# Kernel tuning notes

Measured on AMD Instinct MI355X. Metric: run time of the kernel, lower is better.

Reference implementation:

```python
import jax, jax.numpy as jnp
import numpy as np
import math

B, C, T = 32, 512, 1024
QUERY_DIM = 512
SCALE = 1.0 / math.sqrt(QUERY_DIM)


def setup_inputs() -> dict:
    key = jax.random.key(0)
    ks = jax.random.split(key, 10)
    lim = 1.0 / math.sqrt(C)  # torch Linear default init range
    return {
        "x": jax.random.normal(ks[0], (B, C, T), dtype=jnp.float32),
        "g_query": jax.random.uniform(ks[1], (B, C, T), dtype=jnp.float32),
        "g_keys": jax.random.uniform(ks[2], (B, C, T), dtype=jnp.float32),
        "g_values": jax.random.uniform(ks[3], (B, C, T), dtype=jnp.float32),
        "Wq": jax.random.uniform(ks[4], (C, C), jnp.float32, -lim, lim),
        "bq": jax.random.uniform(ks[5], (C,), jnp.float32, -lim, lim),
        "Wk": jax.random.uniform(ks[6], (C, C), jnp.float32, -lim, lim),
        "bk": jax.random.uniform(ks[7], (C,), jnp.float32, -lim, lim),
        "Wv": jax.random.uniform(ks[8], (C, C), jnp.float32, -lim, lim),
        "bv": jax.random.uniform(ks[9], (C,), jnp.float32, -lim, lim),
    }


def reference(x, g_query, g_keys, g_values, Wq, bq, Wk, bk, Wv, bv):
    # x, gates: [B, C, T] -> transpose to [B, T, C]
    xt = jnp.swapaxes(x, 1, 2)
    gq = jnp.swapaxes(g_query, 1, 2)
    gk = jnp.swapaxes(g_keys, 1, 2)
    gv = jnp.swapaxes(g_values, 1, 2)
    # torch Linear: y = x @ W^T + b
    q = gq * (jnp.einsum('btc,dc->btd', xt, Wq) + bq)  # [B, T, C]
    k = gk * (jnp.einsum('btc,dc->btd', xt, Wk) + bk)  # [B, T, C]
    v = gv * (jnp.einsum('btc,dc->btd', xt, Wv) + bv)  # [B, T, C]
    # energy[b,c,d] = sum_t q[b,t,c] * k[b,t,d]  (channel-channel attention)
    energy = jnp.einsum('btc,btd->bcd', q, k)  # [B, C, C]
    attn = jax.nn.softmax(energy * SCALE, axis=2)
    # out[b,c,t] = sum_d attn[b,c,d] * v[b,t,d]
    out = jnp.einsum('bcd,btd->bct', attn, v)  # [B, C, T]
    return out
```

## Files before the change

kernel.cpp:

```cpp
#include <hip/hip_runtime.h>
#include <math.h>


#define B_ 32
#define C_ 512
#define T_ 1024
#define TC_ ((size_t)524288)
#define CC_ ((size_t)262144)
#define SCALE_ 0.04419417382415922f

typedef short bf16x8 __attribute__((ext_vector_type(8)));
typedef float f32x4 __attribute__((ext_vector_type(4)));

__device__ __forceinline__ unsigned short f2b(float f) {
    unsigned int u = __float_as_uint(f);
    u += 0x7fff + ((u >> 16) & 1);
    return (unsigned short)(u >> 16);
}
__device__ __forceinline__ float b2f(unsigned short h) {
    return __uint_as_float(((unsigned int)h) << 16);
}

#define GLDS(gp, lp) __builtin_amdgcn_global_load_lds( \
    (const __attribute__((address_space(1))) unsigned int*)(const void*)(gp), \
    (__attribute__((address_space(3))) unsigned int*)(void*)(lp), 16, 0, 0)

template<int M, int N, int K, int EP>
__global__ __launch_bounds__(256, 2) void gemm_nt(
    const unsigned short* __restrict__ Ahi, const unsigned short* __restrict__ Alo, size_t sA,
    const unsigned short* __restrict__ Bhi, const unsigned short* __restrict__ Blo, size_t sB,
    float* __restrict__ Cf, size_t sCf,
    unsigned short* __restrict__ Chi, unsigned short* __restrict__ Clo, size_t sC,
    const float* __restrict__ gate, size_t sG,
    const float* __restrict__ bias)
{
    __shared__ __attribute__((aligned(16))) unsigned short sAh[128 * 32];
    __shared__ __attribute__((aligned(16))) unsigned short sAl[128 * 32];
    __shared__ __attribute__((aligned(16))) unsigned short sBh[128 * 32];
    __shared__ __attribute__((aligned(16))) unsigned short sBl[128 * 32];

    const int tid  = threadIdx.x;
    const int lane = tid & 63;
    const int wave = tid >> 6;
    const int bz   = blockIdx.z;
    const int m0   = blockIdx.y * 128;
    const int n0   = blockIdx.x * 128;

    const unsigned short* pAh = Ahi + (size_t)bz * sA;
    const unsigned short* pAl = Alo + (size_t)bz * sA;
    const unsigned short* pBh = Bhi + (size_t)bz * sB;
    const unsigned short* pBl = Blo + (size_t)bz * sB;

    const int srow = wave * 32;
    const int lr   = lane >> 2;
    const int lk   = (lane & 3) * 8;
    const size_t gA0 = (size_t)(m0 + srow + lr) * K + lk;
    const size_t gA1 = (size_t)(m0 + srow + 16 + lr) * K + lk;
    const size_t gB0 = (size_t)(n0 + srow + lr) * K + lk;
    const size_t gB1 = (size_t)(n0 + srow + 16 + lr) * K + lk;
    unsigned short* lds0 = nullptr;  (void)lds0;

    const int wm = (wave & 1) * 64;
    const int wn = (wave >> 1) * 64;
    const int fr = lane & 15;
    const int fk = (lane >> 4) * 8;

    f32x4 acc[4][4] = {};

    for (int k0 = 0; k0 < K; k0 += 32) {
        GLDS(pAh + gA0 + k0, &sAh[srow * 32]);
        GLDS(pAh + gA1 + k0, &sAh[(srow + 16) * 32]);
        GLDS(pAl + gA0 + k0, &sAl[srow * 32]);
        GLDS(pAl + gA1 + k0, &sAl[(srow + 16) * 32]);
        GLDS(pBh + gB0 + k0, &sBh[srow * 32]);
        GLDS(pBh + gB1 + k0, &sBh[(srow + 16) * 32]);
        GLDS(pBl + gB0 + k0, &sBl[srow * 32]);
        GLDS(pBl + gB1 + k0, &sBl[(srow + 16) * 32]);
        __syncthreads();

        bf16x8 aH[4], aL[4], bH[4], bL[4];
        #pragma unroll
        for (int i = 0; i < 4; ++i) {
            int ar = (wm + i * 16 + fr) * 32 + fk;
            int br = (wn + i * 16 + fr) * 32 + fk;
            aH[i] = *(const bf16x8*)(const void*)&sAh[ar];
            aL[i] = *(const bf16x8*)(const void*)&sAl[ar];
            bH[i] = *(const bf16x8*)(const void*)&sBh[br];
            bL[i] = *(const bf16x8*)(const void*)&sBl[br];
        }
        #pragma unroll
        for (int mi = 0; mi < 4; ++mi)
            #pragma unroll
            for (int ni = 0; ni < 4; ++ni) {
                acc[mi][ni] = __builtin_amdgcn_mfma_f32_16x16x32_bf16(aL[mi], bH[ni], acc[mi][ni], 0, 0, 0);
                acc[mi][ni] = __builtin_amdgcn_mfma_f32_16x16x32_bf16(aH[mi], bL[ni], acc[mi][ni], 0, 0, 0);
                acc[mi][ni] = __builtin_amdgcn_mfma_f32_16x16x32_bf16(aH[mi], bH[ni], acc[mi][ni], 0, 0, 0);
            }
        __syncthreads();
    }

    #pragma unroll
    for (int mi = 0; mi < 4; ++mi) {
        #pragma unroll
        for (int r = 0; r < 4; ++r) {
            int m = m0 + wm + mi * 16 + (lane >> 4) * 4 + r;
            #pragma unroll
            for (int ni = 0; ni < 4; ++ni) {
                int n = n0 + wn + ni * 16 + fr;
                float v = acc[mi][ni][r];
                size_t idx = (size_t)m * N + n;
                if (EP == 0 || EP == 1) {
                    float g = gate[(size_t)bz * sG + idx];
                    float val = g * (v + bias[EP == 0 ? m : n]);
                    unsigned short h = f2b(val);
                    Chi[(size_t)bz * sC + idx] = h;
                    Clo[(size_t)bz * sC + idx] = f2b(val - b2f(h));
                } else if (EP == 2) {
                    Cf[(size_t)bz * sCf + idx] = v * SCALE_;
                } else {
                    Cf[(size_t)bz * sCf + idx] = v;
                }
            }
        }
    }
}

__global__ __launch_bounds__(256) void transpose_split(
    const float* __restrict__ x, const float* __restrict__ gv,
    unsigned short* __restrict__ xThi, unsigned short* __restrict__ xTlo,
    float* __restrict__ gvT, int bc, int b_off)
{
    __shared__ float s[64][65];
    const int z = blockIdx.z;
    const int job = z / bc, bz = z % bc;
    const int t0 = blockIdx.x * 64, c0 = blockIdx.y * 64;
    const float* src = (job ? gv : x) + (size_t)(b_off + bz) * TC_;
    const int col = threadIdx.x & 63, rb = threadIdx.x >> 6;

    #pragma unroll
    for (int i = 0; i < 64; i += 4)
        s[i + rb][col] = src[(size_t)(c0 + i + rb) * T_ + t0 + col];
    __syncthreads();

    const size_t ob = (size_t)bz * TC_;
    #pragma unroll
    for (int i = 0; i < 64; i += 4) {
        int tr = i + rb;
        float v = s[col][tr];
        size_t o = ob + (size_t)(t0 + tr) * C_ + c0 + col;
        if (job == 0) {
            unsigned short h = f2b(v);
            xThi[o] = h;
            xTlo[o] = f2b(v - b2f(h));
        } else {
            gvT[o] = v;
        }
    }
}

__global__ __launch_bounds__(256) void split_mat(
    const float* __restrict__ W, unsigned short* __restrict__ hi,
    unsigned short* __restrict__ lo, int n)
{
    int i = blockIdx.x * 256 + threadIdx.x;
    if (i < n) {
        float v = W[i];
        unsigned short h = f2b(v);
        hi[i] = h;
        lo[i] = f2b(v - b2f(h));
    }
}

__global__ __launch_bounds__(256) void softmax_split(
    const float* __restrict__ E, unsigned short* __restrict__ Ahi,
    unsigned short* __restrict__ Alo)
{
    const int row = blockIdx.x;
    const float* p = E + (size_t)row * C_;
    const int tid = threadIdx.x;

    float v0 = p[tid], v1 = p[tid + 256];
    float m = fmaxf(v0, v1);
    #pragma unroll
    for (int off = 32; off > 0; off >>= 1)
        m = fmaxf(m, __shfl_down(m, off, 64));

    __shared__ float sm[4];
    if ((tid & 63) == 0) sm[tid >> 6] = m;
    __syncthreads();
    float M = fmaxf(fmaxf(sm[0], sm[1]), fmaxf(sm[2], sm[3]));

    float e0 = expf(v0 - M), e1 = expf(v1 - M);
    float s = e0 + e1;
    #pragma unroll
    for (int off = 32; off > 0; off >>= 1)
        s += __shfl_down(s, off, 64);

    __shared__ float ss[4];
    if ((tid & 63) == 0) ss[tid >> 6] = s;
    __syncthreads();
    float inv = 1.0f / (ss[0] + ss[1] + ss[2] + ss[3]);

    float a0 = e0 * inv, a1 = e1 * inv;
    size_t o = (size_t)row * C_ + tid;
    unsigned short h0 = f2b(a0);
    Ahi[o] = h0;  Alo[o] = f2b(a0 - b2f(h0));
    unsigned short h1 = f2b(a1);
    Ahi[o + 256] = h1;  Alo[o + 256] = f2b(a1 - b2f(h1));
}

extern "C" void kernel_launch(void* const* d_in, const int* in_sizes, int n_in,
                              void* d_out, int out_size, void* d_ws, size_t ws_size,
                              hipStream_t stream) {
    const float* x  = (const float*)d_in[0];
    const float* gq = (const float*)d_in[1];
    const float* gk = (const float*)d_in[2];
    const float* gv = (const float*)d_in[3];
    const float* Wq = (const float*)d_in[4];
    const float* bq = (const float*)d_in[5];
    const float* Wk = (const float*)d_in[6];
    const float* bk = (const float*)d_in[7];
    const float* Wv = (const float*)d_in[8];
    const float* bv = (const float*)d_in[9];
    float* out = (float*)d_out;

    const size_t wBytes = 6 * CC_ * 2;
    const size_t perBatch = 2 * TC_ * 2 + TC_ * 4 + 6 * TC_ * 2
                          + CC_ * 4 + 2 * CC_ * 2;
    int bc = 1;
    for (int cand = B_; cand >= 1; cand >>= 1)
        if (wBytes + (size_t)cand * perBatch <= ws_size) { bc = cand; break; }

    char* p = (char*)d_ws;
    auto take = [&](size_t bytes) { char* r = p; p += bytes; return r; };
    unsigned short* Wqh = (unsigned short*)take(CC_ * 2);
    unsigned short* Wql = (unsigned short*)take(CC_ * 2);
    unsigned short* Wkh = (unsigned short*)take(CC_ * 2);
    unsigned short* Wkl = (unsigned short*)take(CC_ * 2);
    unsigned short* Wvh = (unsigned short*)take(CC_ * 2);
    unsigned short* Wvl = (unsigned short*)take(CC_ * 2);
    unsigned short* xThi = (unsigned short*)take((size_t)bc * TC_ * 2);
    unsigned short* xTlo = (unsigned short*)take((size_t)bc * TC_ * 2);
    float*          gvT  = (float*)take((size_t)bc * TC_ * 4);
    unsigned short* Qh = (unsigned short*)take((size_t)bc * TC_ * 2);
    unsigned short* Ql = (unsigned short*)take((size_t)bc * TC_ * 2);
    unsigned short* Kh = (unsigned short*)take((size_t)bc * TC_ * 2);
    unsigned short* Kl = (unsigned short*)take((size_t)bc * TC_ * 2);
    unsigned short* Vh = (unsigned short*)take((size_t)bc * TC_ * 2);
    unsigned short* Vl = (unsigned short*)take((size_t)bc * TC_ * 2);
    float*          E  = (float*)take((size_t)bc * CC_ * 4);
    unsigned short* Ah = (unsigned short*)take((size_t)bc * CC_ * 2);
    unsigned short* Al = (unsigned short*)take((size_t)bc * CC_ * 2);

    dim3 blk(256);
    split_mat<<<(int)(CC_ / 256), blk, 0, stream>>>(Wq, Wqh, Wql, (int)CC_);
    split_mat<<<(int)(CC_ / 256), blk, 0, stream>>>(Wk, Wkh, Wkl, (int)CC_);
    split_mat<<<(int)(CC_ / 256), blk, 0, stream>>>(Wv, Wvh, Wvl, (int)CC_);

    for (int b_off = 0; b_off < B_; b_off += bc) {
        transpose_split<<<dim3(T_ / 64, C_ / 64, 2 * bc), blk, 0, stream>>>(
            x, gv, xThi, xTlo, gvT, bc, b_off);

        gemm_nt<512, 1024, 512, 0><<<dim3(8, 4, bc), blk, 0, stream>>>(
            Wqh, Wql, 0, xThi, xTlo, TC_, nullptr, 0, Qh, Ql, TC_,
            gq + (size_t)b_off * TC_, TC_, bq);
        gemm_nt<512, 1024, 512, 0><<<dim3(8, 4, bc), blk, 0, stream>>>(
            Wkh, Wkl, 0, xThi, xTlo, TC_, nullptr, 0, Kh, Kl, TC_,
            gk + (size_t)b_off * TC_, TC_, bk);
        gemm_nt<1024, 512, 512, 1><<<dim3(4, 8, bc), blk, 0, stream>>>(
            xThi, xTlo, TC_, Wvh, Wvl, 0, nullptr, 0, Vh, Vl, TC_,
            gvT, TC_, bv);
        gemm_nt<512, 512, 1024, 2><<<dim3(4, 4, bc), blk, 0, stream>>>(
            Qh, Ql, TC_, Kh, Kl, TC_, E, CC_, nullptr, nullptr, 0, nullptr, 0, nullptr);
        softmax_split<<<dim3(bc * C_), blk, 0, stream>>>(E, Ah, Al);
        gemm_nt<512, 1024, 512, 3><<<dim3(8, 4, bc), blk, 0, stream>>>(
            Ah, Al, CC_, Vh, Vl, TC_, out + (size_t)b_off * TC_, TC_,
            nullptr, nullptr, 0, nullptr, 0, nullptr);
    }
}
```

Before: 676.7 us.

## Double-buffer LDS tiles to overlap global loads with MFMA compute

Splits the shared-memory tiles into two buffers and issues the next K-slice's global-to-LDS loads before computing on the current slice. This halves the number of synchronisation points per K step pair and is meant to hide global memory latency behind the split-bf16 MFMA work. It doubles LDS use to 64KB per block, which may reduce occupancy below the two blocks per CU requested by the launch bounds. It also assumes K is a multiple of 64.

```diff
diff --git a/kernel.cpp b/kernel.cpp
--- a/kernel.cpp
+++ b/kernel.cpp
@@ -34,10 +34,10 @@
     const float* __restrict__ gate, size_t sG,
     const float* __restrict__ bias)
 {
-    __shared__ __attribute__((aligned(16))) unsigned short sAh[128 * 32];
-    __shared__ __attribute__((aligned(16))) unsigned short sAl[128 * 32];
-    __shared__ __attribute__((aligned(16))) unsigned short sBh[128 * 32];
-    __shared__ __attribute__((aligned(16))) unsigned short sBl[128 * 32];
+    __shared__ __attribute__((aligned(16))) unsigned short sAh[2][128 * 32];
+    __shared__ __attribute__((aligned(16))) unsigned short sAl[2][128 * 32];
+    __shared__ __attribute__((aligned(16))) unsigned short sBh[2][128 * 32];
+    __shared__ __attribute__((aligned(16))) unsigned short sBl[2][128 * 32];
 
     const int tid  = threadIdx.x;
     const int lane = tid & 63;
@@ -58,7 +58,6 @@
     const size_t gA1 = (size_t)(m0 + srow + 16 + lr) * K + lk;
     const size_t gB0 = (size_t)(n0 + srow + lr) * K + lk;
     const size_t gB1 = (size_t)(n0 + srow + 16 + lr) * K + lk;
-    unsigned short* lds0 = nullptr;  (void)lds0;
 
     const int wm = (wave & 1) * 64;
     const int wn = (wave >> 1) * 64;
@@ -67,37 +66,52 @@
 
     f32x4 acc[4][4] = {};
 
-    for (int k0 = 0; k0 < K; k0 += 32) {
-        GLDS(pAh + gA0 + k0, &sAh[srow * 32]);
-        GLDS(pAh + gA1 + k0, &sAh[(srow + 16) * 32]);
-        GLDS(pAl + gA0 + k0, &sAl[srow * 32]);
-        GLDS(pAl + gA1 + k0, &sAl[(srow + 16) * 32]);
-        GLDS(pBh + gB0 + k0, &sBh[srow * 32]);
-        GLDS(pBh + gB1 + k0, &sBh[(srow + 16) * 32]);
-        GLDS(pBl + gB0 + k0, &sBl[srow * 32]);
-        GLDS(pBl + gB1 + k0, &sBl[(srow + 16) * 32]);
+#define STAGE(b, koff) do { \
+    GLDS(pAh + gA0 + (koff), &sAh[b][srow * 32]); \
+    GLDS(pAh + gA1 + (koff), &sAh[b][(srow + 16) * 32]); \
+    GLDS(pAl + gA0 + (koff), &sAl[b][srow * 32]); \
+    GLDS(pAl + gA1 + (koff), &sAl[b][(srow + 16) * 32]); \
+    GLDS(pBh + gB0 + (koff), &sBh[b][srow * 32]); \
+    GLDS(pBh + gB1 + (koff), &sBh[b][(srow + 16) * 32]); \
+    GLDS(pBl + gB0 + (koff), &sBl[b][srow * 32]); \
+    GLDS(pBl + gB1 + (koff), &sBl[b][(srow + 16) * 32]); \
+} while (0)
+
+#define COMPUTE(b) do { \
+    bf16x8 aH[4], aL[4], bH[4], bL[4]; \
+    _Pragma("unroll") \
+    for (int i = 0; i < 4; ++i) { \
+        int ar = (wm + i * 16 + fr) * 32 + fk; \
+        int br = (wn + i * 16 + fr) * 32 + fk; \
+        aH[i] = *(const bf16x8*)(const void*)&sAh[b][ar]; \
+        aL[i] = *(const bf16x8*)(const void*)&sAl[b][ar]; \
+        bH[i] = *(const bf16x8*)(const void*)&sBh[b][br]; \
+        bL[i] = *(const bf16x8*)(const void*)&sBl[b][br]; \
+    } \
+    _Pragma("unroll") \
+    for (int mi = 0; mi < 4; ++mi) \
+        _Pragma("unroll") \
+        for (int ni = 0; ni < 4; ++ni) { \
+            acc[mi][ni] = __builtin_amdgcn_mfma_f32_16x16x32_bf16(aL[mi], bH[ni], acc[mi][ni], 0, 0, 0); \
+            acc[mi][ni] = __builtin_amdgcn_mfma_f32_16x16x32_bf16(aH[mi], bL[ni], acc[mi][ni], 0, 0, 0); \
+            acc[mi][ni] = __builtin_amdgcn_mfma_f32_16x16x32_bf16(aH[mi], bH[ni], acc[mi][ni], 0, 0, 0); \
+        } \
+} while (0)
+
+    STAGE(0, 0);
+    __syncthreads();
+
+    for (int k0 = 0; k0 < K; k0 += 64) {
+        STAGE(1, k0 + 32);
+        COMPUTE(0);
         __syncthreads();
-
-        bf16x8 aH[4], aL[4], bH[4], bL[4];
-        #pragma unroll
-        for (int i = 0; i < 4; ++i) {
-            int ar = (wm + i * 16 + fr) * 32 + fk;
-            int br = (wn + i * 16 + fr) * 32 + fk;
-            aH[i] = *(const bf16x8*)(const void*)&sAh[ar];
-            aL[i] = *(const bf16x8*)(const void*)&sAl[ar];
-            bH[i] = *(const bf16x8*)(const void*)&sBh[br];
-            bL[i] = *(const bf16x8*)(const void*)&sBl[br];
-        }
-        #pragma unroll
-        for (int mi = 0; mi < 4; ++mi)
-            #pragma unroll
-            for (int ni = 0; ni < 4; ++ni) {
-                acc[mi][ni] = __builtin_amdgcn_mfma_f32_16x16x32_bf16(aL[mi], bH[ni], acc[mi][ni], 0, 0, 0);
-                acc[mi][ni] = __builtin_amdgcn_mfma_f32_16x16x32_bf16(aH[mi], bL[ni], acc[mi][ni], 0, 0, 0);
-                acc[mi][ni] = __builtin_amdgcn_mfma_f32_16x16x32_bf16(aH[mi], bH[ni], acc[mi][ni], 0, 0, 0);
-            }
+        if (k0 + 64 < K) STAGE(0, k0 + 64);
+        COMPUTE(1);
         __syncthreads();
     }
+
+#undef STAGE
+#undef COMPUTE
 
     #pragma unroll
     for (int mi = 0; mi < 4; ++mi) {
```

Result: no change. 688.1 us (+1.7%).
